# Performance work log

Measured on AMD Instinct MI355X. Metric: run time of the kernel, lower is better.

The kernel has to match this reference:

```python
import jax, jax.numpy as jnp
import numpy as np


def _lstm_cell(x, h, c, Wih, Whh, b):
    # torch gate order: input, forget, cell(g), output
    gates = x @ Wih.T + h @ Whh.T + b  # [B, 4H]
    i, f, g, o = jnp.split(gates, 4, axis=-1)
    i = jax.nn.sigmoid(i)
    f = jax.nn.sigmoid(f)
    g = jnp.tanh(g)
    o = jax.nn.sigmoid(o)
    c = f * c + i * g
    return o * jnp.tanh(c), c


def setup_inputs() -> dict:
    key = jax.random.key(0)
    ks = jax.random.split(key, 20)
    B, Te, Td, X, H = 4096, 168, 24, 8, 64
    s = 0.1  # weight scale for numerical sanity in the AR sampling loop
    return {
        "enc_x": jax.random.normal(ks[0], (B, Te, X), jnp.float32),
        "enc_z": jax.random.uniform(ks[1], (B, Te, 1), jnp.float32),
        "dec_x": jax.random.normal(ks[2], (B, Td, X - 1), jnp.float32),
        "v": jax.random.uniform(ks[3], (B, 1, 1), jnp.float32) + 0.5,  # positive scale
        "eps": jax.random.normal(ks[4], (B, Td, 1), jnp.float32),
        "W_ih0": s * jax.random.normal(ks[5], (4 * H, X), jnp.float32),
        "W_hh0": s * jax.random.normal(ks[6], (4 * H, H), jnp.float32),
        "b0": s * jax.random.normal(ks[7], (4 * H,), jnp.float32),
        "W_ih1": s * jax.random.normal(ks[8], (4 * H, H), jnp.float32),
        "W_hh1": s * jax.random.normal(ks[9], (4 * H, H), jnp.float32),
        "b1": s * jax.random.normal(ks[10], (4 * H,), jnp.float32),
        "W_ih2": s * jax.random.normal(ks[11], (4 * H, H), jnp.float32),
        "W_hh2": s * jax.random.normal(ks[12], (4 * H, H), jnp.float32),
        "b2": s * jax.random.normal(ks[13], (4 * H,), jnp.float32),
        "w_m": s * jax.random.normal(ks[14], (H, 1), jnp.float32),
        "b_m": jnp.zeros((1,), jnp.float32),
        "w_a": s * jax.random.normal(ks[15], (H, 1), jnp.float32),
        "b_a": jnp.zeros((1,), jnp.float32),
    }


def reference(enc_x, enc_z, dec_x, v, eps,
              W_ih0, W_hh0, b0, W_ih1, W_hh1, b1, W_ih2, W_hh2, b2,
              w_m, b_m, w_a, b_a):
    B = enc_x.shape[0]
    H = W_hh0.shape[1]

    def step3(x, h, c):
        h0, c0 = _lstm_cell(x, h[0], c[0], W_ih0, W_hh0, b0)
        h1, c1 = _lstm_cell(h0, h[1], c[1], W_ih1, W_hh1, b1)
        h2, c2 = _lstm_cell(h1, h[2], c[2], W_ih2, W_hh2, b2)
        return (h0, h1, h2), (c0, c1, c2), h2

    z0 = jnp.zeros((B, H), enc_x.dtype)
    h = (z0, z0, z0)
    c = (z0, z0, z0)

    # ---- encoder: 3-layer LSTM over Te steps ----
    def enc_step(carry, x_t):
        h, c = carry
        h, c, _ = step3(x_t, h, c)
        return (h, c), None

    (h, c), _ = jax.lax.scan(enc_step, (h, c), jnp.swapaxes(enc_x, 0, 1))

    vf = v[:, 0, :]                 # [B, 1]
    z = enc_z[:, -1, :] / vf        # [B, 1]

    def dec_step(carry, inp):
        h, c, z = carry
        x_t, e_t = inp              # [B, X-1], [B, 1]
        x = jnp.concatenate([z, x_t], axis=-1)   # [B, X]
        h, c, o = step3(x, h, c)
        m = (o @ w_m + b_m) * vf                  # Gaussian mean, rescaled
        a = jax.nn.softplus(o @ w_a + b_a) * vf   # Gaussian std, rescaled
        zs = m + a * e_t                          # reparameterized sample
        return (h, c, zs / vf), zs

    xs = (jnp.swapaxes(dec_x, 0, 1), jnp.swapaxes(eps, 0, 1))
    _, Z = jax.lax.scan(dec_step, (h, c, z), xs)  # [Td, B, 1]
    return jnp.swapaxes(Z, 0, 1)                  # [B, Td, 1]
```

## Files before the change

### kernel.cpp

```cpp
#include <hip/hip_runtime.h>
#include <math.h>

#define B_TOT 4096
#define TE 168
#define TD 24
#define NWG 256
#define HSTR 72

typedef _Float16 f16;
typedef __attribute__((ext_vector_type(8))) _Float16 f16x8;
typedef __attribute__((ext_vector_type(4))) float f32x4;

#define SCL_S (-1.4426950408889634f)
#define SCL_G (2.885390081777927f)

__global__ __launch_bounds__(256) void pack_kernel(
    const float* __restrict__ Wih0, const float* __restrict__ Whh0,
    const float* __restrict__ Wih1, const float* __restrict__ Whh1,
    const float* __restrict__ Wih2, const float* __restrict__ Whh2,
    f16* __restrict__ pk)
{
    int idx = blockIdx.x * 256 + threadIdx.x;
    int j = idx & 7;
    int t = idx >> 3;
    int ln = t & 63; t >>= 6;
    int c  = t & 3;  t >>= 2;
    int q  = t & 3;  t >>= 2;
    int l  = t % 3;
    int w  = t / 3;
    int row = q * 64 + w * 16 + (ln & 15);
    int k   = c * 32 + ((ln >> 4) << 3) + j;
    float val = 0.f;
    if (l == 0) {
        if (k < 8)                 val = Wih0[row * 8 + k];
        else if (k >= 32 && k < 96) val = Whh0[row * 64 + (k - 32)];
    } else if (l == 1) {
        val = (k < 64) ? Wih1[row * 64 + k] : Whh1[row * 64 + (k - 64)];
    } else {
        val = (k < 64) ? Wih2[row * 64 + k] : Whh2[row * 64 + (k - 64)];
    }
    const float sc = (q == 2) ? SCL_G : SCL_S;
    pk[idx] = (f16)(val * sc);
}

__device__ __forceinline__ float softplusf(float x) { return fmaxf(x, 0.f) + log1pf(__expf(-fabsf(x))); }

__global__ __launch_bounds__(768, 3) void lstm_kernel(
    const float* __restrict__ enc_x, const float* __restrict__ enc_z,
    const float* __restrict__ dec_x, const float* __restrict__ v,
    const float* __restrict__ eps,   const f16* __restrict__ pk,
    const float* __restrict__ b0, const float* __restrict__ b1,
    const float* __restrict__ b2,
    const float* __restrict__ w_m, const float* __restrict__ b_m,
    const float* __restrict__ w_a, const float* __restrict__ b_a,
    float* __restrict__ out)
{
    const int tid  = threadIdx.x;
    const int lane = tid & 63;
    const int wv   = (tid >> 6) & 3;
    const int role = tid >> 8;
    const int bg   = blockIdx.x * 16;
    const int m16  = lane & 15;
    const int quad = lane >> 4;

    __shared__ f16  hbuf[2][3][16][HSTR];
    __shared__ f16  xbuf[2][16][32];
    __shared__ float zbuf[16];

    {
        uint* hz = (uint*)&hbuf[0][0][0][0];
        const int HW = 2 * 3 * 16 * HSTR / 2;
        for (int i = tid; i < HW; i += 768) hz[i] = 0u;
        uint* xz = (uint*)&xbuf[0][0][0];
        for (int i = tid; i < 512; i += 768) xz[i] = 0u;
    }

    f16x8 wgt[4][4];
#define PKOFF(l, q, c) ((((((size_t)wv * 3 + (l)) * 4 + (q)) * 4 + (c)) * 64 + lane) * 8)
    {
        const f16* pkr = pk + PKOFF(role, 0, 0);
#pragma unroll
        for (int q = 0; q < 4; ++q)
#pragma unroll
            for (int c = 0; c < 4; ++c)
                wgt[c][q] = *(const f16x8*)(pkr + (q * 4 + c) * 64 * 8);
    }
#undef PKOFF

    const int hid_self = wv * 16 + m16;
    f32x4 bsp[4];
    {
        const float* bp = (role == 0) ? b0 : (role == 1) ? b1 : b2;
#pragma unroll
        for (int q = 0; q < 4; ++q) {
            const float sc = (q == 2) ? SCL_G : SCL_S;
            float bv = bp[q * 64 + hid_self] * sc;
            bsp[q] = (f32x4){bv, bv, bv, bv};
        }
    }

    f16* hb = &hbuf[0][0][0][0];
    const int aoff = m16 * HSTR + quad * 8;
    float cst[4] = {};

#define HBASE(pp, l) (hb + ((pp) * 3 + (l)) * (16 * HSTR))
#define MFMA16(af, bf, cf) __builtin_amdgcn_mfma_f32_16x16x32_f16(af, bf, cf, 0, 0, 0)

#define MM_F(P, aptr, wi)                                                     \
    {                                                                         \
        f16x8 af = *(const f16x8*)(aptr);                                     \
        P##0 = MFMA16(af, wgt[wi][0], bsp[0]);                                \
        P##1 = MFMA16(af, wgt[wi][1], bsp[1]);                                \
        P##2 = MFMA16(af, wgt[wi][2], bsp[2]);                                \
        P##3 = MFMA16(af, wgt[wi][3], bsp[3]);                                \
    }
#define MM(P, aptr, wi)                                                       \
    {                                                                         \
        f16x8 af = *(const f16x8*)(aptr);                                     \
        P##0 = MFMA16(af, wgt[wi][0], P##0);                                  \
        P##1 = MFMA16(af, wgt[wi][1], P##1);                                  \
        P##2 = MFMA16(af, wgt[wi][2], P##2);                                  \
        P##3 = MFMA16(af, wgt[wi][3], P##3);                                  \
    }

#define CELL(P, lh, PP)                                                       \
    {                                                                         \
        f16* hw = HBASE(PP, lh) + hid_self;                                   \
        _Pragma("unroll")                                                     \
        for (int r = 0; r < 4; ++r) {                                         \
            float Ei = __builtin_amdgcn_exp2f(P##0[r]);                       \
            float Ef = __builtin_amdgcn_exp2f(P##1[r]);                       \
            float Eg = __builtin_amdgcn_exp2f(P##2[r]);                       \
            float Eo = __builtin_amdgcn_exp2f(P##3[r]);                       \
            float ef1 = 1.f + Ef;                                             \
            float pig = (1.f + Ei) * (1.f + Eg);                              \
            float R   = __builtin_amdgcn_rcpf(pig * ef1);                     \
            float fv  = pig * R;                                              \
            float ig  = (Eg - 1.f) * ef1 * R;                                 \
            float cn  = fmaf(fv, cst[r], ig);                                 \
            cst[r] = cn;                                                      \
            float Ec  = __builtin_amdgcn_exp2f(cn * SCL_G);                   \
            float Roc = __builtin_amdgcn_rcpf((1.f + Eo) * (1.f + Ec));       \
            hw[(quad * 4 + r) * HSTR] = (f16)((Ec - 1.f) * Roc);              \
        }                                                                     \
    }

    const int  sidx = tid - 512;
    const bool isst = (sidx >= 0) && (sidx < 128);
    const int  mS = (sidx >> 3) & 15, kS = sidx & 7;
    const float* xrow = enc_x + ((size_t)(bg + mS) * TE) * 8 + kS;

#define ROUND(PP, D0, D1, D2, DS, DP, T0)                                     \
    {                                                                         \
        __syncthreads();                                                      \
        f32x4 a0, a1, a2, a3;                                                 \
        if (role == 0) {                                                      \
            if (D0) {                                                         \
                MM_F(a, &xbuf[PP][0][0] + m16 * 32 + quad * 8, 0);            \
                MM(a, HBASE(1 - (PP), 0) + aoff,      1);                     \
                MM(a, HBASE(1 - (PP), 0) + aoff + 32, 2);                     \
                CELL(a, 0, PP);                                               \
            }                                                                 \
        } else if (role == 1) {                                               \
            if (D1) {                                                         \
                MM_F(a, HBASE(1 - (PP), 0) + aoff,      0);                   \
                MM(a, HBASE(1 - (PP), 0) + aoff + 32, 1);                     \
                MM(a, HBASE(1 - (PP), 1) + aoff,      2);                     \
                MM(a, HBASE(1 - (PP), 1) + aoff + 32, 3);                     \
                CELL(a, 1, PP);                                               \
            }                                                                 \
        } else {                                                              \
            if (D2) {                                                         \
                MM_F(a, HBASE(1 - (PP), 1) + aoff,      0);                   \
                MM(a, HBASE(1 - (PP), 1) + aoff + 32, 1);                     \
                MM(a, HBASE(1 - (PP), 2) + aoff,      2);                     \
                MM(a, HBASE(1 - (PP), 2) + aoff + 32, 3);                     \
            }                                                                 \
            if (DS && isst) {                                                 \
                xbuf[1 - (PP)][mS][kS] = (f16)xpre;                           \
                if (DP) xpre = xrow[((T0) + 2) * 8];                          \
            }                                                                 \
            if (D2) CELL(a, 2, PP);                                           \
        }                                                                     \
    }

    __syncthreads();

    float xpre = 0.f;
    if (isst) {
        xbuf[0][mS][kS] = (f16)xrow[0];
        xpre = xrow[8];
    }
    ROUND(0, 1, 0, 0, 1, 1, 0)
    ROUND(1, 1, 1, 0, 1, 1, 1)
    for (int t = 2; t < 166; t += 2) {
        ROUND(0, 1, 1, 1, 1, 1, t)
        ROUND(1, 1, 1, 1, 1, 1, t + 1)
    }
    ROUND(0, 1, 1, 1, 1, 0, 166)
    ROUND(1, 1, 1, 1, 0, 0, 167)
    ROUND(0, 0, 1, 1, 0, 0, 168)
    ROUND(1, 0, 0, 1, 0, 0, 169)

    const int   mH = (tid >> 4) & 15;
    const float vf = (role == 0) ? v[bg + mH] : 0.f;
    float wmr[4], war[4];
#pragma unroll
    for (int r = 0; r < 4; ++r) {
        wmr[r] = w_m[(tid & 15) + 16 * r];
        war[r] = w_a[(tid & 15) + 16 * r];
    }
    const float bmv = b_m[0], bav = b_a[0];
    if (role == 0 && (tid & 15) == 0)
        zbuf[mH] = enc_z[(size_t)(bg + mH) * TE + (TE - 1)] / vf;

#define DEC_STEP(PA, t)                                                       \
    {                                                                         \
        __syncthreads();                           \
        if (isst) {                                                           \
            float xv = (kS == 0) ? zbuf[mS]                                   \
                                 : dec_x[((size_t)(bg + mS) * TD + (t)) * 7 + (kS - 1)]; \
            xbuf[PA][mS][kS] = (f16)xv;                                       \
        }                                                                     \
        __syncthreads();                                       \
        f32x4 a0, a1, a2, a3;                                                 \
        if (role == 0) {                                                      \
            MM_F(a, &xbuf[PA][0][0] + m16 * 32 + quad * 8, 0);                \
            MM(a, HBASE(1 - (PA), 0) + aoff,      1);                         \
            MM(a, HBASE(1 - (PA), 0) + aoff + 32, 2);                         \
            CELL(a, 0, PA);                                                   \
        }                                                                     \
        __syncthreads();                                  \
        if (role == 1) {                                                      \
            MM_F(a, HBASE(PA, 0) + aoff,      0);                             \
            MM(a, HBASE(PA, 0) + aoff + 32, 1);                               \
            MM(a, HBASE(PA, 1) + aoff,      2);                               \
            MM(a, HBASE(PA, 1) + aoff + 32, 3);                               \
            CELL(a, 1, 1 - (PA));                                             \
        }                                                                     \
        __syncthreads();                                \
        if (role == 2) {                                                      \
            MM_F(a, HBASE(1 - (PA), 1) + aoff,      0);                       \
            MM(a, HBASE(1 - (PA), 1) + aoff + 32, 1);                         \
            MM(a, HBASE(1 - (PA), 2) + aoff,      2);                         \
            MM(a, HBASE(1 - (PA), 2) + aoff + 32, 3);                         \
            CELL(a, 2, PA);                                                   \
        }                                                                     \
        __syncthreads();                                  \
        if (role == 0) {                                                      \
            float sm = 0.f, sa = 0.f;                                         \
            const f16* h2p = HBASE(PA, 2) + mH * HSTR;                        \
            _Pragma("unroll")                                                 \
            for (int r = 0; r < 4; ++r) {                                     \
                float hv = (float)h2p[(tid & 15) + 16 * r];                   \
                sm += hv * wmr[r];                                            \
                sa += hv * war[r];                                            \
            }                                                                 \
            _Pragma("unroll")                                                 \
            for (int off = 1; off < 16; off <<= 1) {                          \
                sm += __shfl_xor(sm, off, 64);                                \
                sa += __shfl_xor(sa, off, 64);                                \
            }                                                                 \
            if ((tid & 15) == 0) {                                            \
                float mo  = (sm + bmv) * vf;                                  \
                float ao  = softplusf(sa + bav) * vf;                         \
                float zsv = mo + ao * eps[(size_t)(bg + mH) * TD + (t)];      \
                out[(size_t)(bg + mH) * TD + (t)] = zsv;                      \
                zbuf[mH] = zsv / vf;                                          \
            }                                                                 \
        }                                                                     \
    }

    for (int t = 0; t < TD; t += 2) {
        DEC_STEP(0, t)
        DEC_STEP(1, t + 1)
    }

#undef HBASE
#undef MFMA16
#undef MM_F
#undef MM
#undef CELL
#undef ROUND
#undef DEC_STEP
}

extern "C" void kernel_launch(void* const* d_in, const int* in_sizes, int n_in,
                              void* d_out, int out_size, void* d_ws, size_t ws_size,
                              hipStream_t stream) {
    const float* enc_x = (const float*)d_in[0];
    const float* enc_z = (const float*)d_in[1];
    const float* dec_x = (const float*)d_in[2];
    const float* v     = (const float*)d_in[3];
    const float* eps   = (const float*)d_in[4];
    const float* Wih0  = (const float*)d_in[5];
    const float* Whh0  = (const float*)d_in[6];
    const float* b0    = (const float*)d_in[7];
    const float* Wih1  = (const float*)d_in[8];
    const float* Whh1  = (const float*)d_in[9];
    const float* b1    = (const float*)d_in[10];
    const float* Wih2  = (const float*)d_in[11];
    const float* Whh2  = (const float*)d_in[12];
    const float* b2    = (const float*)d_in[13];
    const float* w_m   = (const float*)d_in[14];
    const float* b_m   = (const float*)d_in[15];
    const float* w_a   = (const float*)d_in[16];
    const float* b_a   = (const float*)d_in[17];
    float* out = (float*)d_out;
    f16*   pk  = (f16*)d_ws;

    pack_kernel<<<384, 256, 0, stream>>>(Wih0, Whh0, Wih1, Whh1, Wih2, Whh2, pk);
    lstm_kernel<<<NWG, 768, 0, stream>>>(enc_x, enc_z, dec_x, v, eps, pk,
                                         b0, b1, b2, w_m, b_m, w_a, b_a, out);
}
```

Measured before the change: 310.7 us.

## Replace encoder barriers with LDS counter dataflow between layer wave groups

The encoder's lock-step wavefront rounds, which called __syncthreads every step, are replaced by per-layer LDS atomic counters with spin-waits. Each layer role can now run ahead of the next by up to NB-1 steps, using a 4-deep ring of h buffers. Layer 0 now reads enc_x straight into registers instead of going through the xbuf staging path. The aim is to remove block-wide barrier stalls and let the layers pipeline freely, at the cost of busy-wait polling on LDS and some fragile memory ordering.

```diff
diff --git a/kernel.cpp b/kernel.cpp
--- a/kernel.cpp
+++ b/kernel.cpp
@@ -6,6 +6,7 @@
 #define TD 24
 #define NWG 256
 #define HSTR 72
+#define NB 4
 
 typedef _Float16 f16;
 typedef __attribute__((ext_vector_type(8))) _Float16 f16x8;
@@ -45,6 +46,15 @@
 
 __device__ __forceinline__ float softplusf(float x) { return fmaxf(x, 0.f) + log1pf(__expf(-fabsf(x))); }
 
+__device__ __forceinline__ void wait_ge(volatile int* c, int tgt, int& seen) {
+    if (seen < tgt) {
+        int v;
+        do { v = *c; } while (v < tgt);
+        seen = v;
+        asm volatile("" ::: "memory");
+    }
+}
+
 __global__ __launch_bounds__(768, 3) void lstm_kernel(
     const float* __restrict__ enc_x, const float* __restrict__ enc_z,
     const float* __restrict__ dec_x, const float* __restrict__ v,
@@ -63,16 +73,18 @@
     const int m16  = lane & 15;
     const int quad = lane >> 4;
 
-    __shared__ f16  hbuf[2][3][16][HSTR];
-    __shared__ f16  xbuf[2][16][32];
+    __shared__ f16   hbuf[NB][3][16][HSTR];
+    __shared__ f16   xbuf[2][16][32];
     __shared__ float zbuf[16];
+    __shared__ int   cnt[3];
 
     {
         uint* hz = (uint*)&hbuf[0][0][0][0];
-        const int HW = 2 * 3 * 16 * HSTR / 2;
+        const int HW = NB * 3 * 16 * HSTR / 2;
         for (int i = tid; i < HW; i += 768) hz[i] = 0u;
         uint* xz = (uint*)&xbuf[0][0][0];
         for (int i = tid; i < 512; i += 768) xz[i] = 0u;
+        if (tid < 3) cnt[tid] = 0;
     }
 
     f16x8 wgt[4][4];
@@ -103,9 +115,16 @@
     const int aoff = m16 * HSTR + quad * 8;
     float cst[4] = {};
 
-#define HBASE(pp, l) (hb + ((pp) * 3 + (l)) * (16 * HSTR))
+#define HBASE(bf, l) (hb + ((bf) * 3 + (l)) * (16 * HSTR))
 #define MFMA16(af, bf, cf) __builtin_amdgcn_mfma_f32_16x16x32_f16(af, bf, cf, 0, 0, 0)
 
+#define MM_R(P, areg, wi)                                                     \
+    {                                                                         \
+        P##0 = MFMA16(areg, wgt[wi][0], bsp[0]);                              \
+        P##1 = MFMA16(areg, wgt[wi][1], bsp[1]);                              \
+        P##2 = MFMA16(areg, wgt[wi][2], bsp[2]);                              \
+        P##3 = MFMA16(areg, wgt[wi][3], bsp[3]);                              \
+    }
 #define MM_F(P, aptr, wi)                                                     \
     {                                                                         \
         f16x8 af = *(const f16x8*)(aptr);                                     \
@@ -123,9 +142,9 @@
         P##3 = MFMA16(af, wgt[wi][3], P##3);                                  \
     }
 
-#define CELL(P, lh, PP)                                                       \
-    {                                                                         \
-        f16* hw = HBASE(PP, lh) + hid_self;                                   \
+#define CELL(P, lh, BF)                                                       \
+    {                                                                         \
+        f16* hw = HBASE(BF, lh) + hid_self;                                   \
         _Pragma("unroll")                                                     \
         for (int r = 0; r < 4; ++r) {                                         \
             float Ei = __builtin_amdgcn_exp2f(P##0[r]);                       \
@@ -145,62 +164,77 @@
         }                                                                     \
     }
 
+#define SIGNAL(i)                                                             \
+    {                                                                         \
+        asm volatile("s_waitcnt lgkmcnt(0)" ::: "memory");                    \
+        atomicAdd((int*)&cnt[i], 1);                                          \
+    }
+
+    __syncthreads();
+
+    if (role == 0) {
+        const float* xp = enc_x + (size_t)(bg + m16) * (TE * 8);
+        f32x4 xa = {}, xb = {};
+        if (quad == 0) { xa = *(const f32x4*)xp; xb = *(const f32x4*)(xp + 4); }
+        int s0 = 0, s1 = 0;
+        for (int t = 0; t < TE; ++t) {
+            wait_ge(&cnt[0], 4 * t, s0);
+            wait_ge(&cnt[1], 4 * (t - (NB - 1)), s1);
+            f16x8 af = {};
+            if (quad == 0) {
+#pragma unroll
+                for (int j = 0; j < 4; ++j) { af[j] = (f16)xa[j]; af[4 + j] = (f16)xb[j]; }
+                if (t + 1 < TE) {
+                    xa = *(const f32x4*)(xp + (size_t)(t + 1) * 8);
+                    xb = *(const f32x4*)(xp + (size_t)(t + 1) * 8 + 4);
+                }
+            }
+            f32x4 a0, a1, a2, a3;
+            MM_R(a, af, 0);
+            const f16* h0p = HBASE((t + NB - 1) & (NB - 1), 0) + aoff;
+            MM(a, h0p, 1);
+            MM(a, h0p + 32, 2);
+            CELL(a, 0, t & (NB - 1));
+            SIGNAL(0);
+        }
+    } else if (role == 1) {
+        int s0 = 0, s1 = 0, s2 = 0;
+        for (int t = 0; t < TE; ++t) {
+            wait_ge(&cnt[0], 4 * (t + 1), s0);
+            wait_ge(&cnt[1], 4 * t, s1);
+            wait_ge(&cnt[2], 4 * (t - (NB - 1)), s2);
+            const f16* h0p = HBASE(t & (NB - 1), 0) + aoff;
+            const f16* h1p = HBASE((t + NB - 1) & (NB - 1), 1) + aoff;
+            f32x4 a0, a1, a2, a3;
+            MM_F(a, h0p, 0);
+            MM(a, h0p + 32, 1);
+            MM(a, h1p, 2);
+            MM(a, h1p + 32, 3);
+            CELL(a, 1, t & (NB - 1));
+            SIGNAL(1);
+        }
+    } else {
+        int s1 = 0, s2 = 0;
+        for (int t = 0; t < TE; ++t) {
+            wait_ge(&cnt[1], 4 * (t + 1), s1);
+            wait_ge(&cnt[2], 4 * t, s2);
+            const f16* h1p = HBASE(t & (NB - 1), 1) + aoff;
+            const f16* h2p = HBASE((t + NB - 1) & (NB - 1), 2) + aoff;
+            f32x4 a0, a1, a2, a3;
+            MM_F(a, h1p, 0);
+            MM(a, h1p + 32, 1);
+            MM(a, h2p, 2);
+            MM(a, h2p + 32, 3);
+            CELL(a, 2, t & (NB - 1));
+            SIGNAL(2);
+        }
+    }
+
+    __syncthreads();
+
     const int  sidx = tid - 512;
     const bool isst = (sidx >= 0) && (sidx < 128);
     const int  mS = (sidx >> 3) & 15, kS = sidx & 7;
-    const float* xrow = enc_x + ((size_t)(bg + mS) * TE) * 8 + kS;
-
-#define ROUND(PP, D0, D1, D2, DS, DP, T0)                                     \
-    {                                                                         \
-        __syncthreads();                                                      \
-        f32x4 a0, a1, a2, a3;                                                 \
-        if (role == 0) {                                                      \
-            if (D0) {                                                         \
-                MM_F(a, &xbuf[PP][0][0] + m16 * 32 + quad * 8, 0);            \
-                MM(a, HBASE(1 - (PP), 0) + aoff,      1);                     \
-                MM(a, HBASE(1 - (PP), 0) + aoff + 32, 2);                     \
-                CELL(a, 0, PP);                                               \
-            }                                                                 \
-        } else if (role == 1) {                                               \
-            if (D1) {                                                         \
-                MM_F(a, HBASE(1 - (PP), 0) + aoff,      0);                   \
-                MM(a, HBASE(1 - (PP), 0) + aoff + 32, 1);                     \
-                MM(a, HBASE(1 - (PP), 1) + aoff,      2);                     \
-                MM(a, HBASE(1 - (PP), 1) + aoff + 32, 3);                     \
-                CELL(a, 1, PP);                                               \
-            }                                                                 \
-        } else {                                                              \
-            if (D2) {                                                         \
-                MM_F(a, HBASE(1 - (PP), 1) + aoff,      0);                   \
-                MM(a, HBASE(1 - (PP), 1) + aoff + 32, 1);                     \
-                MM(a, HBASE(1 - (PP), 2) + aoff,      2);                     \
-                MM(a, HBASE(1 - (PP), 2) + aoff + 32, 3);                     \
-            }                                                                 \
-            if (DS && isst) {                                                 \
-                xbuf[1 - (PP)][mS][kS] = (f16)xpre;                           \
-                if (DP) xpre = xrow[((T0) + 2) * 8];                          \
-            }                                                                 \
-            if (D2) CELL(a, 2, PP);                                           \
-        }                                                                     \
-    }
-
-    __syncthreads();
-
-    float xpre = 0.f;
-    if (isst) {
-        xbuf[0][mS][kS] = (f16)xrow[0];
-        xpre = xrow[8];
-    }
-    ROUND(0, 1, 0, 0, 1, 1, 0)
-    ROUND(1, 1, 1, 0, 1, 1, 1)
-    for (int t = 2; t < 166; t += 2) {
-        ROUND(0, 1, 1, 1, 1, 1, t)
-        ROUND(1, 1, 1, 1, 1, 1, t + 1)
-    }
-    ROUND(0, 1, 1, 1, 1, 0, 166)
-    ROUND(1, 1, 1, 1, 0, 0, 167)
-    ROUND(0, 0, 1, 1, 0, 0, 168)
-    ROUND(1, 0, 0, 1, 0, 0, 169)
 
     const int   mH = (tid >> 4) & 15;
     const float vf = (role == 0) ? v[bg + mH] : 0.f;
@@ -214,42 +248,44 @@
     if (role == 0 && (tid & 15) == 0)
         zbuf[mH] = enc_z[(size_t)(bg + mH) * TE + (TE - 1)] / vf;
 
-#define DEC_STEP(PA, t)                                                       \
-    {                                                                         \
+#define DEC_STEP(t)                                                           \
+    {                                                                         \
+        const int bc = (t) & (NB - 1);                                        \
+        const int bp = ((t) + NB - 1) & (NB - 1);                             \
         __syncthreads();                           \
         if (isst) {                                                           \
             float xv = (kS == 0) ? zbuf[mS]                                   \
                                  : dec_x[((size_t)(bg + mS) * TD + (t)) * 7 + (kS - 1)]; \
-            xbuf[PA][mS][kS] = (f16)xv;                                       \
+            xbuf[(t) & 1][mS][kS] = (f16)xv;                                  \
         }                                                                     \
         __syncthreads();                                       \
         f32x4 a0, a1, a2, a3;                                                 \
         if (role == 0) {                                                      \
-            MM_F(a, &xbuf[PA][0][0] + m16 * 32 + quad * 8, 0);                \
-            MM(a, HBASE(1 - (PA), 0) + aoff,      1);                         \
-            MM(a, HBASE(1 - (PA), 0) + aoff + 32, 2);                         \
-            CELL(a, 0, PA);                                                   \
-        }                                                                     \
-        __syncthreads();                                  \
+            MM_F(a, &xbuf[(t) & 1][0][0] + m16 * 32 + quad * 8, 0);           \
+            MM(a, HBASE(bp, 0) + aoff,      1);                               \
+            MM(a, HBASE(bp, 0) + aoff + 32, 2);                               \
+            CELL(a, 0, bc);                                                   \
+        }                                                                     \
+        __syncthreads();                                      \
         if (role == 1) {                                                      \
-            MM_F(a, HBASE(PA, 0) + aoff,      0);                             \
-            MM(a, HBASE(PA, 0) + aoff + 32, 1);                               \
-            MM(a, HBASE(PA, 1) + aoff,      2);                               \
-            MM(a, HBASE(PA, 1) + aoff + 32, 3);                               \
-            CELL(a, 1, 1 - (PA));                                             \
-        }                                                                     \
-        __syncthreads();                                \
+            MM_F(a, HBASE(bc, 0) + aoff,      0);                             \
+            MM(a, HBASE(bc, 0) + aoff + 32, 1);                               \
+            MM(a, HBASE(bp, 1) + aoff,      2);                               \
+            MM(a, HBASE(bp, 1) + aoff + 32, 3);                               \
+            CELL(a, 1, bc);                                                   \
+        }                                                                     \
+        __syncthreads();                                      \
         if (role == 2) {                                                      \
-            MM_F(a, HBASE(1 - (PA), 1) + aoff,      0);                       \
-            MM(a, HBASE(1 - (PA), 1) + aoff + 32, 1);                         \
-            MM(a, HBASE(1 - (PA), 2) + aoff,      2);                         \
-            MM(a, HBASE(1 - (PA), 2) + aoff + 32, 3);                         \
-            CELL(a, 2, PA);                                                   \
-        }                                                                     \
-        __syncthreads();                                  \
+            MM_F(a, HBASE(bc, 1) + aoff,      0);                             \
+            MM(a, HBASE(bc, 1) + aoff + 32, 1);                               \
+            MM(a, HBASE(bp, 2) + aoff,      2);                               \
+            MM(a, HBASE(bp, 2) + aoff + 32, 3);                               \
+            CELL(a, 2, bc);                                                   \
+        }                                                                     \
+        __syncthreads();                                      \
         if (role == 0) {                                                      \
             float sm = 0.f, sa = 0.f;                                         \
-            const f16* h2p = HBASE(PA, 2) + mH * HSTR;                        \
+            const f16* h2p = HBASE(bc, 2) + mH * HSTR;                        \
             _Pragma("unroll")                                                 \
             for (int r = 0; r < 4; ++r) {                                     \
                 float hv = (float)h2p[(tid & 15) + 16 * r];                   \
@@ -271,17 +307,17 @@
         }                                                                     \
     }
 
-    for (int t = 0; t < TD; t += 2) {
-        DEC_STEP(0, t)
-        DEC_STEP(1, t + 1)
+    for (int t = 0; t < TD; ++t) {
+        DEC_STEP(t)
     }
 
 #undef HBASE
 #undef MFMA16
+#undef MM_R
 #undef MM_F
 #undef MM
 #undef CELL
-#undef ROUND
+#undef SIGNAL
 #undef DEC_STEP
 }
 
```

Result: slower. 325.4 us (+4.8%).
